# Kernel optimization log

Hardware: AMD Instinct MI355X
Metric: run time of the kernel (lower is better)

The kernel has to match this reference:

```python
import jax, jax.numpy as jnp
import numpy as np

B, P, ENC, DEC, ATT, EMB, V, CAPLEN = 128, 196, 2048, 512, 512, 300, 10000, 51


def setup_inputs() -> dict:
    key = jax.random.key(0)
    ks = jax.random.split(key, 20)
    s = 0.02
    lens = jax.random.randint(ks[2], (B, 1), 2, CAPLEN + 1)
    lens = lens.at[0, 0].set(CAPLEN)  # ensure max decode length == CAPLEN-1 (static T)
    return {
        'encoder_out': jax.random.normal(ks[0], (B, P, ENC), jnp.float32),
        'encoded_captions': jax.random.randint(ks[1], (B, CAPLEN), 0, V),
        'caption_lengths': lens,
        'W_enc_att': jax.random.normal(ks[3], (ATT, ENC)) * s,
        'b_enc_att': jnp.zeros((ATT,)),
        'W_dec_att': jax.random.normal(ks[4], (ATT, DEC)) * s,
        'b_dec_att': jnp.zeros((ATT,)),
        'w_full_att': jax.random.normal(ks[5], (ATT,)) * s,
        'b_full_att': jnp.zeros(()),
        'embedding': jax.random.uniform(ks[6], (V, EMB), minval=-0.1, maxval=0.1),
        'W_ih': jax.random.normal(ks[7], (4 * DEC, EMB + ENC)) * s,
        'b_ih': jnp.zeros((4 * DEC,)),
        'W_hh': jax.random.normal(ks[8], (4 * DEC, DEC)) * s,
        'b_hh': jnp.zeros((4 * DEC,)),
        'W_init_h': jax.random.normal(ks[9], (DEC, ENC)) * s,
        'b_init_h': jnp.zeros((DEC,)),
        'W_init_c': jax.random.normal(ks[10], (DEC, ENC)) * s,
        'b_init_c': jnp.zeros((DEC,)),
        'W_fbeta': jax.random.normal(ks[11], (ENC, DEC)) * s,
        'b_fbeta': jnp.zeros((ENC,)),
        'W_fc': jax.random.uniform(ks[12], (V, DEC), minval=-0.1, maxval=0.1),
        'b_fc': jnp.zeros((V,)),
    }


def reference(encoder_out, encoded_captions, caption_lengths,
              W_enc_att, b_enc_att, W_dec_att, b_dec_att, w_full_att, b_full_att,
              embedding, W_ih, b_ih, W_hh, b_hh,
              W_init_h, b_init_h, W_init_c, b_init_c,
              W_fbeta, b_fbeta, W_fc, b_fc):
    lens = caption_lengths[:, 0]
    sort_ind = jnp.argsort(-lens)                      # descending length sort
    lens_s = lens[sort_ind]
    enc = encoder_out[sort_ind]                        # [B,P,ENC]
    caps = encoded_captions[sort_ind]                  # [B,CAPLEN]
    emb = embedding[caps]                              # [B,CAPLEN,EMB]
    mean_enc = enc.mean(axis=1)
    h0 = mean_enc @ W_init_h.T + b_init_h
    c0 = mean_enc @ W_init_c.T + b_init_c
    att1 = enc @ W_enc_att.T + b_enc_att               # precomputed [B,P,ATT]
    decode_lengths = lens_s - 1
    T = caps.shape[1] - 1                              # static max decode length
    mask = jnp.arange(T)[:, None] < decode_lengths[None, :]   # [T,B]
    emb_t = jnp.transpose(emb[:, :T, :], (1, 0, 2))    # [T,B,EMB]

    def step(carry, xs):
        h, c = carry
        e_t, m_t = xs
        att2 = h @ W_dec_att.T + b_dec_att             # [B,ATT]
        score = jnp.einsum('bpa,a->bp', jax.nn.relu(att1 + att2[:, None, :]), w_full_att) + b_full_att
        alpha = jax.nn.softmax(score, axis=1)          # [B,P]
        awe = jnp.einsum('bp,bpe->be', alpha, enc)     # [B,ENC]
        gate = jax.nn.sigmoid(h @ W_fbeta.T + b_fbeta)
        awe = gate * awe
        x = jnp.concatenate([e_t, awe], axis=1)        # [B,EMB+ENC]
        gates = x @ W_ih.T + b_ih + h @ W_hh.T + b_hh
        i, f, g, o = jnp.split(gates, 4, axis=1)
        i, f, o = jax.nn.sigmoid(i), jax.nn.sigmoid(f), jax.nn.sigmoid(o)
        g = jnp.tanh(g)
        c_new = f * c + i * g
        h_new = o * jnp.tanh(c_new)
        m = m_t[:, None]
        # state only advances for still-active (length > t) rows
        h2 = jnp.where(m, h_new, h)
        c2 = jnp.where(m, c_new, c)
        preds = h_new @ W_fc.T + b_fc                  # dropout is identity in eval
        preds = jnp.where(m, preds, 0.0)
        alpha = jnp.where(m, alpha, 0.0)
        return (h2, c2), (preds, alpha)

    (_, _), (preds, alphas) = jax.lax.scan(step, (h0, c0), (emb_t, mask))
    predictions = jnp.transpose(preds, (1, 0, 2))      # [B,T,V]
    alphas = jnp.transpose(alphas, (1, 0, 2))          # [B,T,P]
    return predictions, caps, decode_lengths, alphas, sort_ind
```

## Files before the change

kernel.cpp:

```cpp
#include <hip/hip_runtime.h>
#include <math.h>

#define B 128
#define PP 196
#define ENC 2048
#define DEC 512
#define ATTD 512
#define EMB 300
#define VV 10000
#define CAPLEN 51
#define TT 50
#define KPAD 2880
#define NPPAD 10112

static const long long OFF_PRED = 0LL;
static const long long OFF_CAPS = 64000000LL;
static const long long OFF_DECL = 64006528LL;
static const long long OFF_ALPH = 64006656LL;
static const long long OFF_SORT = 65261056LL;

typedef unsigned short ushort_t;
typedef unsigned int uint_t;
typedef short bf8 __attribute__((ext_vector_type(8)));
typedef float f4 __attribute__((ext_vector_type(4)));

__device__ __forceinline__ float sigf(float x){ return 1.f/(1.f+expf(-x)); }
__device__ __forceinline__ float b2f(ushort_t u){
  union{uint_t i; float f;} v; v.i = ((uint_t)u)<<16; return v.f;
}
__device__ __forceinline__ ushort_t f2b(float f){
  union{float f; uint_t i;} v; v.f = f;
  uint_t r = v.i + 0x7fffu + ((v.i>>16)&1u);
  return (ushort_t)(r>>16);
}
__device__ __forceinline__ uint_t pack2(float lo, float hi){
  return (uint_t)f2b(lo) | ((uint_t)f2b(hi)<<16);
}
__device__ __forceinline__ float2 b2x2(uint_t u){
  union{uint_t i; float f;} a,b; a.i = u<<16; b.i = u & 0xffff0000u;
  return make_float2(a.f, b.f);
}

__device__ __forceinline__ void gemm128x64(
    const ushort_t* __restrict__ Ab, int lda, int m0,
    const ushort_t* __restrict__ Bb, int ldb, int n0,
    int Kbeg, int Kend, int mbound,
    ushort_t* As, ushort_t* Bs, int tid, f4 acc[4][2])
{
  const int r = tid>>2, cby = (tid&3)*8;
  const int w = tid>>6, l = tid&63;
  const int wm = w>>1, wn = w&1, lr = l&15, lk = (l>>4)*8;
  uint4 qa0 = *(const uint4*)(Ab + (size_t)(m0+r)*lda    + Kbeg + cby);
  uint4 qa1 = *(const uint4*)(Ab + (size_t)(m0+64+r)*lda + Kbeg + cby);
  uint4 qb  = *(const uint4*)(Bb + (size_t)(n0+r)*ldb    + Kbeg + cby);
  for (int k0=Kbeg; k0<Kend; k0+=32){
    __syncthreads();
    *(uint4*)(As + r*40      + cby) = qa0;
    *(uint4*)(As + (64+r)*40 + cby) = qa1;
    *(uint4*)(Bs + r*40      + cby) = qb;
    __syncthreads();
    if (k0+32 < Kend){
      qa0 = *(const uint4*)(Ab + (size_t)(m0+r)*lda    + k0+32 + cby);
      qa1 = *(const uint4*)(Ab + (size_t)(m0+64+r)*lda + k0+32 + cby);
      qb  = *(const uint4*)(Bb + (size_t)(n0+r)*ldb    + k0+32 + cby);
    }
    bf8 b0 = *(const bf8*)(Bs + (wn*32+lr)*40    + lk);
    bf8 b1 = *(const bf8*)(Bs + (wn*32+16+lr)*40 + lk);
    #pragma unroll
    for (int fm=0; fm<4; fm++){
      if (wm*64 + fm*16 < mbound){
        bf8 a = *(const bf8*)(As + (wm*64+fm*16+lr)*40 + lk);
        acc[fm][0] = __builtin_amdgcn_mfma_f32_16x16x32_bf16(a, b0, acc[fm][0], 0, 0, 0);
        acc[fm][1] = __builtin_amdgcn_mfma_f32_16x16x32_bf16(a, b1, acc[fm][1], 0, 0, 0);
      }
    }
  }
}

__global__ __launch_bounds__(128) void k_prep(const int* __restrict__ cap_len,
    const int* __restrict__ enc_caps, float* __restrict__ out,
    int* __restrict__ sort_i, int* __restrict__ decl_i, int* __restrict__ caps_i,
    int* __restrict__ nact_d){
  __shared__ int lens[B];
  __shared__ int sind[B];
  __shared__ int s_dl[B];
  int t = threadIdx.x;
  lens[t] = cap_len[t];
  __syncthreads();
  int my = lens[t];
  int rank = 0;
  for (int j=0;j<B;j++){
    int lj = lens[j];
    if (lj > my || (lj == my && j < t)) rank++;
  }
  sind[rank] = t;
  __syncthreads();
  int src = sind[t];
  sort_i[t] = src;
  int dl = lens[src]-1;
  decl_i[t] = dl;
  s_dl[t] = dl;
  out[OFF_DECL+t] = (float)dl;
  out[OFF_SORT+t] = (float)src;
  for (int j=0;j<CAPLEN;j++){
    int v = enc_caps[src*CAPLEN+j];
    caps_i[t*CAPLEN+j] = v;
    out[OFF_CAPS + t*CAPLEN + j] = (float)v;
  }
  __syncthreads();
  if (t < TT){
    int cnt = 0;
    for (int b2=0;b2<B;b2++) cnt += (s_dl[b2] > t) ? 1 : 0;
    nact_d[t] = cnt;
  }
}

__global__ __launch_bounds__(256) void k_mean(const float* __restrict__ enc,
    const int* __restrict__ sort_i, float* __restrict__ meanb){
  int b = blockIdx.x;
  int e = blockIdx.y*256 + threadIdx.x;
  int sb = sort_i[b];
  const float* p0 = enc + (size_t)sb*PP*ENC + e;
  float s = 0.f;
  for (int p=0;p<PP;p++) s += p0[(size_t)p*ENC];
  meanb[b*ENC+e] = s * (1.0f/PP);
}

__global__ __launch_bounds__(256) void k_init(const float* __restrict__ meanb,
    const float* __restrict__ Wh, const float* __restrict__ bh,
    const float* __restrict__ Wc, const float* __restrict__ bc,
    float* __restrict__ h, float* __restrict__ c, ushort_t* __restrict__ xb_s){
  __shared__ float aT[64*132];
  __shared__ float wT[64*36];
  int tid = threadIdx.x;
  int n0 = blockIdx.x*32;
  const float* Wm  = blockIdx.y ? Wc : Wh;
  const float* bia = blockIdx.y ? bc : bh;
  float* dst = blockIdx.y ? c : h;
  int bt = tid&15, nt = tid>>4;
  float acc[8][2] = {};
  for (int k0=0;k0<ENC;k0+=64){
    for (int idx=tid; idx<64*128; idx+=256){
      int k=idx&63, m=idx>>6;
      aT[k*132+m] = meanb[m*ENC + k0+k];
    }
    for (int idx=tid; idx<64*32; idx+=256){
      int k=idx&63, n=idx>>6;
      wT[k*36+n] = Wm[(size_t)(n0+n)*ENC + k0+k];
    }
    __syncthreads();
    #pragma unroll 4
    for (int k=0;k<64;k++){
      float a[8], wv[2];
      *(float4*)&a[0] = *(const float4*)&aT[k*132+bt*8];
      *(float4*)&a[4] = *(const float4*)&aT[k*132+bt*8+4];
      *(float2*)&wv[0] = *(const float2*)&wT[k*36+nt*2];
      #pragma unroll
      for (int i=0;i<8;i++){ acc[i][0]+=a[i]*wv[0]; acc[i][1]+=a[i]*wv[1]; }
    }
    __syncthreads();
  }
  #pragma unroll
  for (int i=0;i<8;i++){
    int m = bt*8+i;
    #pragma unroll
    for (int j=0;j<2;j++){
      int n = n0+nt*2+j;
      float v = acc[i][j] + bia[n];
      dst[m*DEC+n] = v;
      if (blockIdx.y == 0) xb_s[(size_t)m*KPAD + n] = f2b(v);
    }
  }
}

__global__ __launch_bounds__(256) void k_wkb(const float* __restrict__ Whh,
    const float* __restrict__ Wih, uint_t* __restrict__ wkb_u){
  int n = blockIdx.x;
  int j = n>>2, g = n&3;
  int rrow = g*512 + j;
  uint_t* dst = wkb_u + (size_t)n*(KPAD/2);
  for (int u=threadIdx.x; u<KPAD/2; u+=256){
    int k = 2*u; float a, bvl;
    if (k < 512){ float2 v = *(const float2*)(Whh + (size_t)rrow*512 + k); a=v.x; bvl=v.y; }
    else if (k < 2860){ float2 v = *(const float2*)(Wih + (size_t)rrow*2348 + (k-512)); a=v.x; bvl=v.y; }
    else { a=0.f; bvl=0.f; }
    dst[u] = pack2(a, bvl);
  }
}
__global__ __launch_bounds__(256) void k_wcatb(const float* __restrict__ Wda,
    const float* __restrict__ Wfb, uint_t* __restrict__ wcat_u){
  int n = blockIdx.x;
  const float* src = (n < 512) ? (Wda + (size_t)n*512) : (Wfb + (size_t)(n-512)*512);
  uint_t* dst = wcat_u + (size_t)n*256;
  int u = threadIdx.x;
  float2 v = *(const float2*)(src + 2*u);
  dst[u] = pack2(v.x, v.y);
}
__global__ __launch_bounds__(256) void k_wfcb(const float* __restrict__ Wfc,
    uint_t* __restrict__ wfc_u){
  int n = blockIdx.x;
  uint_t* dst = wfc_u + (size_t)n*256;
  int u = threadIdx.x;
  if (n < VV){
    float2 v = *(const float2*)(Wfc + (size_t)n*512 + 2*u);
    dst[u] = pack2(v.x, v.y);
  } else dst[u] = 0u;
}
__global__ __launch_bounds__(256) void k_weab(const float* __restrict__ Wea,
    uint_t* __restrict__ wea_u){
  int n = blockIdx.x;
  uint_t* dst = wea_u + (size_t)n*1024;
  for (int u=threadIdx.x; u<1024; u+=256){
    float2 v = *(const float2*)(Wea + (size_t)n*2048 + 2*u);
    dst[u] = pack2(v.x, v.y);
  }
}
__global__ __launch_bounds__(160) void k_embb(const float* __restrict__ embedding,
    const int* __restrict__ caps_i, uint_t* __restrict__ embb_u){
  int b = blockIdx.x, t = blockIdx.y, tid = threadIdx.x;
  if (tid >= 150) return;
  int tok = caps_i[b*CAPLEN+t];
  float2 v = *(const float2*)(embedding + (size_t)tok*EMB + 2*tid);
  embb_u[((size_t)b*TT+t)*150 + tid] = pack2(v.x, v.y);
}
__global__ __launch_bounds__(256) void k_xpad(uint_t* __restrict__ xb_u){
  for (int u=threadIdx.x; u<1280; u+=256){
    int r = u/10, cu = u - r*10;
    xb_u[(size_t)r*(KPAD/2) + 1430 + cu] = 0u;
  }
}
__global__ __launch_bounds__(256) void k_encb(const float* __restrict__ enc,
    const int* __restrict__ sort_i, ushort_t* __restrict__ encb){
  int row = blockIdx.x;
  int b = row/PP, p = row - b*PP;
  int sb = sort_i[b];
  const float4* s4 = (const float4*)(enc + ((size_t)sb*PP+p)*ENC);
  uint4* d4 = (uint4*)(encb + (size_t)row*ENC);
  int tid = threadIdx.x;
  float4 f0 = s4[tid*2], f1 = s4[tid*2+1];
  uint4 q;
  q.x = pack2(f0.x,f0.y); q.y = pack2(f0.z,f0.w);
  q.z = pack2(f1.x,f1.y); q.w = pack2(f1.z,f1.w);
  d4[tid] = q;
}

__global__ __launch_bounds__(256) void k_zero(const int* __restrict__ decl_i,
    float* __restrict__ out){
  int blk = blockIdx.x;
  int b = blk/TT, t = blk - b*TT;
  if (t < decl_i[b]) return;
  float4 z = {0.f,0.f,0.f,0.f};
  float4* p = (float4*)(out + OFF_PRED + ((size_t)b*TT+t)*VV);
  for (int i=threadIdx.x; i<VV/4; i+=256) p[i] = z;
  size_t ao = (size_t)OFF_ALPH + ((size_t)b*TT+t)*PP;
  if (threadIdx.x < PP) out[ao + threadIdx.x] = 0.f;
}

__global__ __launch_bounds__(256) void k_att1g(const ushort_t* __restrict__ encb,
    const ushort_t* __restrict__ weab, const float* __restrict__ bea,
    ushort_t* __restrict__ attb){
  __shared__ ushort_t As[128*40];
  __shared__ ushort_t Bs[64*40];
  int tid = threadIdx.x;
  int m0 = blockIdx.x*128, n0 = blockIdx.y*64;
  f4 acc[4][2] = {};
  gemm128x64(encb, 2048, m0, weab, 2048, n0, 0, 2048, 128, As, Bs, tid, acc);
  int w = tid>>6, l = tid&63, wm = w>>1, wn = w&1;
  #pragma unroll
  for (int fm=0; fm<4; fm++)
    #pragma unroll
    for (int fn=0; fn<2; fn++)
      #pragma unroll
      for (int rr=0; rr<4; rr++){
        int m = m0 + wm*64 + fm*16 + (l>>4)*4 + rr;
        int n = n0 + wn*32 + fn*16 + (l&15);
        attb[(size_t)m*ATTD + n] = f2b(acc[fm][fn][rr] + bea[n]);
      }
}

__global__ __launch_bounds__(256) void k_att1_f32(const float* __restrict__ enc,
    const float* __restrict__ Wea, const float* __restrict__ bea,
    const int* __restrict__ sort_i, ushort_t* __restrict__ attb){
  __shared__ float aT[64*132];
  __shared__ float wT[64*68];
  int tid = threadIdx.x;
  int m0 = blockIdx.x*128;
  int n0 = blockIdx.y*64;
  int bt = tid&15, nt = tid>>4;
  float acc[8][4] = {};
  for (int k0=0;k0<ENC;k0+=64){
    for (int idx=tid; idx<64*128; idx+=256){
      int k=idx&63, m=idx>>6;
      int mg = m0+m;
      int b = mg/PP; int p = mg - b*PP;
      int sb = sort_i[b];
      aT[k*132+m] = enc[((size_t)sb*PP + p)*ENC + k0+k];
    }
    for (int idx=tid; idx<64*64; idx+=256){
      int k=idx&63, n=idx>>6;
      wT[k*68+n] = Wea[(size_t)(n0+n)*ENC + k0+k];
    }
    __syncthreads();
    #pragma unroll 4
    for (int k=0;k<64;k++){
      float a[8], wv[4];
      *(float4*)&a[0] = *(const float4*)&aT[k*132+bt*8];
      *(float4*)&a[4] = *(const float4*)&aT[k*132+bt*8+4];
      *(float4*)&wv[0] = *(const float4*)&wT[k*68+nt*4];
      #pragma unroll
      for (int i=0;i<8;i++)
        #pragma unroll
        for (int j=0;j<4;j++) acc[i][j] += a[i]*wv[j];
    }
    __syncthreads();
  }
  #pragma unroll
  for (int i=0;i<8;i++){
    int mg = m0+bt*8+i;
    #pragma unroll
    for (int j=0;j<4;j++){
      int n = n0+nt*4+j;
      attb[(size_t)mg*ATTD + n] = f2b(acc[i][j] + bea[n]);
    }
  }
}

__global__ __launch_bounds__(256) void k_hmats(const ushort_t* __restrict__ xb,
    const ushort_t* __restrict__ wcatb, const float* __restrict__ bda,
    const float* __restrict__ bfb, const int* __restrict__ nact_d,
    float* __restrict__ att2s, float* __restrict__ gate, int t){
  __shared__ ushort_t As[128*40];
  __shared__ ushort_t Bs[64*40];
  int tid = threadIdx.x;
  int n0 = blockIdx.x*64;
  int mb = nact_d[t];
  f4 acc[4][2] = {};
  gemm128x64(xb, KPAD, 0, wcatb, 512, n0, 0, 512, mb, As, Bs, tid, acc);
  int w = tid>>6, l = tid&63, wm = w>>1, wn = w&1;
  #pragma unroll
  for (int fm=0; fm<4; fm++)
    #pragma unroll
    for (int fn=0; fn<2; fn++)
      #pragma unroll
      for (int rr=0; rr<4; rr++){
        int m = wm*64 + fm*16 + (l>>4)*4 + rr;
        int n = n0 + wn*32 + fn*16 + (l&15);
        float v = acc[fm][fn][rr];
        if (n < 512) att2s[m*512+n] = v + bda[n];
        else         gate[m*2048 + (n-512)] = sigf(v + bfb[n-512]);
      }
}

template<bool FULLT>
__global__ __launch_bounds__(512) void k_score_awe(const ushort_t* __restrict__ attb,
    const float* __restrict__ att2s, const float* __restrict__ wfa,
    const float* __restrict__ bfa, const int* __restrict__ decl_i,
    const float* __restrict__ gate, const ushort_t* __restrict__ encb,
    const float* __restrict__ enc, const int* __restrict__ sort_i,
    float* __restrict__ out, uint_t* __restrict__ xb_u,
    const uint_t* __restrict__ embb_u, const float* __restrict__ embedding,
    const int* __restrict__ caps_i, int t){
  int b = blockIdx.x, tid = threadIdx.x;
  if (t >= decl_i[b]) return;
  __shared__ float s_a2[512], s_w[512], s_sc[200], s_al[200], s_red[8], s_red2[8];
  if (FULLT){
    if (tid < 150) xb_u[b*(KPAD/2) + 256 + tid] = embb_u[((size_t)b*TT+t)*150 + tid];
  } else {
    if (tid < 150){
      int tok = caps_i[b*CAPLEN+t];
      float2 e = *(const float2*)(embedding + (size_t)tok*EMB + 2*tid);
      xb_u[b*(KPAD/2) + 256 + tid] = pack2(e.x, e.y);
    }
  }
  s_a2[tid] = att2s[b*512+tid];
  s_w[tid]  = wfa[tid];
  __syncthreads();
  int wid = tid>>6, lane = tid&63;
  float b0 = bfa[0];
  for (int p=wid; p<PP; p+=8){
    uint4 q = ((const uint4*)(attb + ((size_t)b*PP + p)*ATTD))[lane];
    int j = lane*8;
    float2 x0=b2x2(q.x), x1=b2x2(q.y), x2=b2x2(q.z), x3=b2x2(q.w);
    float s = fmaxf(x0.x+s_a2[j+0],0.f)*s_w[j+0] + fmaxf(x0.y+s_a2[j+1],0.f)*s_w[j+1]
            + fmaxf(x1.x+s_a2[j+2],0.f)*s_w[j+2] + fmaxf(x1.y+s_a2[j+3],0.f)*s_w[j+3]
            + fmaxf(x2.x+s_a2[j+4],0.f)*s_w[j+4] + fmaxf(x2.y+s_a2[j+5],0.f)*s_w[j+5]
            + fmaxf(x3.x+s_a2[j+6],0.f)*s_w[j+6] + fmaxf(x3.y+s_a2[j+7],0.f)*s_w[j+7];
    #pragma unroll
    for (int off=32;off;off>>=1) s += __shfl_down(s,off);
    if (lane==0) s_sc[p] = s + b0;
  }
  __syncthreads();
  float sc = (tid<PP) ? s_sc[tid] : -1e30f;
  float mx = sc;
  #pragma unroll
  for (int off=32;off;off>>=1) mx = fmaxf(mx, __shfl_down(mx,off));
  if (lane==0) s_red[wid] = mx;
  __syncthreads();
  mx = s_red[0];
  #pragma unroll
  for (int i=1;i<8;i++) mx = fmaxf(mx, s_red[i]);
  float e = (tid<PP) ? expf(sc-mx) : 0.f;
  float sm = e;
  #pragma unroll
  for (int off=32;off;off>>=1) sm += __shfl_down(sm,off);
  if (lane==0) s_red2[wid] = sm;
  __syncthreads();
  float tot = 0.f;
  #pragma unroll
  for (int i=0;i<8;i++) tot += s_red2[i];
  float inv = 1.f/tot;
  if (tid<PP){
    float al = e*inv;
    s_al[tid] = al;
    out[(size_t)OFF_ALPH + ((size_t)b*TT+t)*PP + tid] = al;
  }
  __syncthreads();
  float a0=0.f,a1=0.f,a2=0.f,a3=0.f;
  if (FULLT){
    const uint2* E = (const uint2*)(encb + (size_t)b*PP*ENC) + tid;
    #pragma unroll 4
    for (int p=0;p<PP;p++){
      float al = s_al[p];
      uint2 q = E[(size_t)p*(ENC/4)];
      float2 u = b2x2(q.x), v = b2x2(q.y);
      a0 += al*u.x; a1 += al*u.y; a2 += al*v.x; a3 += al*v.y;
    }
  } else {
    const float4* E = (const float4*)(enc + (size_t)sort_i[b]*PP*ENC) + tid;
    #pragma unroll 4
    for (int p=0;p<PP;p++){
      float al = s_al[p];
      float4 q = E[(size_t)p*(ENC/4)];
      a0 += al*q.x; a1 += al*q.y; a2 += al*q.z; a3 += al*q.w;
    }
  }
  float4 g = *(const float4*)(gate + b*2048 + tid*4);
  xb_u[b*(KPAD/2) + 406 + tid*2]     = pack2(a0*g.x, a1*g.y);
  xb_u[b*(KPAD/2) + 406 + tid*2 + 1] = pack2(a2*g.z, a3*g.w);
}

__global__ __launch_bounds__(256) void k_b1gf(const ushort_t* __restrict__ xb,
    const ushort_t* __restrict__ wkbi, const float* __restrict__ b_ih,
    const float* __restrict__ b_hh, const int* __restrict__ decl_i,
    const int* __restrict__ nact_d, float* __restrict__ c,
    ushort_t* __restrict__ hnball, ushort_t* __restrict__ xb_s, int t){
  __shared__ ushort_t As[128*40];
  __shared__ ushort_t Bs[64*40];
  __shared__ float sacc[128*68];
  __shared__ float sbias[64];
  __shared__ int s_dl[128];
  int tid = threadIdx.x;
  int n0 = blockIdx.x*64;
  int j0 = n0>>2;
  int mb = nact_d[t];
  if (tid < 64){
    int n = n0 + tid;
    int j = n>>2, g = n&3;
    sbias[tid] = b_ih[g*512+j] + b_hh[g*512+j];
  }
  if (tid < 128) s_dl[tid] = decl_i[tid];
  f4 acc[4][2] = {};
  gemm128x64(xb, KPAD, 0, wkbi, KPAD, n0, 0, KPAD, mb, As, Bs, tid, acc);
  int w = tid>>6, l = tid&63, wm = w>>1, wn = w&1;
  __syncthreads();
  #pragma unroll
  for (int fm=0; fm<4; fm++)
    #pragma unroll
    for (int fn=0; fn<2; fn++)
      #pragma unroll
      for (int rr=0; rr<4; rr++){
        int m = wm*64 + fm*16 + (l>>4)*4 + rr;
        int n = wn*32 + fn*16 + (l&15);
        sacc[m*68+n] = acc[fm][fn][rr];
      }
  __syncthreads();
  #pragma unroll
  for (int q=0; q<8; q++){
    int idx = q*256 + tid;
    int m = idx>>4, u = idx&15;
    int j = j0 + u;
    float gi = sacc[m*68 + u*4+0] + sbias[u*4+0];
    float gf = sacc[m*68 + u*4+1] + sbias[u*4+1];
    float gg = sacc[m*68 + u*4+2] + sbias[u*4+2];
    float go = sacc[m*68 + u*4+3] + sbias[u*4+3];
    float cn = sigf(gf)*c[m*512+j] + sigf(gi)*tanhf(gg);
    float hn = sigf(go)*tanhf(cn);
    hnball[((size_t)t*B + m)*512 + j] = f2b(hn);
    if (t < s_dl[m]){
      c[m*512+j] = cn;
      xb_s[(size_t)m*KPAD + j] = f2b(hn);
    }
  }
}

__global__ __launch_bounds__(256) void k_predall(const ushort_t* __restrict__ hnball,
    const ushort_t* __restrict__ wfcb, const float* __restrict__ b_fc,
    const int* __restrict__ nact_d, float* __restrict__ out){
  __shared__ ushort_t As[128*40];
  __shared__ ushort_t Bs[64*40];
  int tid = threadIdx.x;
  int t = blockIdx.y;
  int n0 = blockIdx.x*64;
  int mb = nact_d[t];
  f4 acc[4][2] = {};
  gemm128x64(hnball + (size_t)t*B*512, 512, 0, wfcb, 512, n0, 0, 512, mb, As, Bs, tid, acc);
  int w = tid>>6, l = tid&63, wm = w>>1, wn = w&1;
  #pragma unroll
  for (int fm=0; fm<4; fm++)
    #pragma unroll
    for (int fn=0; fn<2; fn++)
      #pragma unroll
      for (int rr=0; rr<4; rr++){
        int m = wm*64 + fm*16 + (l>>4)*4 + rr;
        int n = n0 + wn*32 + fn*16 + (l&15);
        if (m < mb && n < VV)
          out[OFF_PRED + ((size_t)m*TT + t)*VV + n] = acc[fm][fn][rr] + b_fc[n];
      }
}

extern "C" void kernel_launch(void* const* d_in, const int* in_sizes, int n_in,
                              void* d_out, int out_size, void* d_ws, size_t ws_size,
                              hipStream_t stream){
  const float* enc       = (const float*)d_in[0];
  const int*   caps_in   = (const int*)d_in[1];
  const int*   caplen    = (const int*)d_in[2];
  const float* W_enc_att = (const float*)d_in[3];
  const float* b_enc_att = (const float*)d_in[4];
  const float* W_dec_att = (const float*)d_in[5];
  const float* b_dec_att = (const float*)d_in[6];
  const float* w_full_att= (const float*)d_in[7];
  const float* b_full_att= (const float*)d_in[8];
  const float* embedding = (const float*)d_in[9];
  const float* W_ih      = (const float*)d_in[10];
  const float* b_ih      = (const float*)d_in[11];
  const float* W_hh      = (const float*)d_in[12];
  const float* b_hh      = (const float*)d_in[13];
  const float* W_init_h  = (const float*)d_in[14];
  const float* b_init_h  = (const float*)d_in[15];
  const float* W_init_c  = (const float*)d_in[16];
  const float* b_init_c  = (const float*)d_in[17];
  const float* W_fbeta   = (const float*)d_in[18];
  const float* b_fbeta   = (const float*)d_in[19];
  const float* W_fc      = (const float*)d_in[20];
  const float* b_fc      = (const float*)d_in[21];
  float* out = (float*)d_out;

  float* W = (float*)d_ws;
  size_t o = 0;
  auto A = [&](size_t n){ float* p = W + o; o += n; return p; };

  bool FULL = ws_size >= 172000000ull;

  float* h      = A(65536);
  float* c      = A(65536);
  float* att2s  = A(65536);
  float* gate   = A(262144);
  float* meanb  = A(262144);
  ushort_t* xb    = (ushort_t*)A(184320);
  ushort_t* wkb   = (ushort_t*)A(2949120);
  ushort_t* wcatb = (ushort_t*)A(655360);
  ushort_t* wfcb  = (ushort_t*)A(2588672);
  ushort_t* hnball= (ushort_t*)A(1638400);
  ushort_t* attb  = (ushort_t*)A(6422528);
  int* ip = (int*)A(6848);
  int* sort_i = ip;
  int* decl_i = ip + 128;
  int* nact_d = ip + 256;
  int* caps_i = ip + 320;
  ushort_t* weab = nullptr;
  uint_t*   embb_u = nullptr;
  ushort_t* encb = nullptr;
  if (FULL){
    weab   = (ushort_t*)A(524288);
    embb_u = (uint_t*)A(960000);
    encb   = (ushort_t*)A(25690112);
  }
  uint_t* xb_u = (uint_t*)xb;

  k_prep<<<1,128,0,stream>>>(caplen, caps_in, out, sort_i, decl_i, caps_i, nact_d);
  k_mean<<<dim3(128,8),256,0,stream>>>(enc, sort_i, meanb);
  k_init<<<dim3(16,2),256,0,stream>>>(meanb, W_init_h, b_init_h, W_init_c, b_init_c, h, c, xb);
  k_wkb<<<2048,256,0,stream>>>(W_hh, W_ih, (uint_t*)wkb);
  k_wcatb<<<2560,256,0,stream>>>(W_dec_att, W_fbeta, (uint_t*)wcatb);
  k_wfcb<<<NPPAD,256,0,stream>>>(W_fc, (uint_t*)wfcb);
  k_xpad<<<1,256,0,stream>>>(xb_u);
  k_zero<<<6400,256,0,stream>>>(decl_i, out);
  if (FULL){
    k_weab<<<512,256,0,stream>>>(W_enc_att, (uint_t*)weab);
    k_embb<<<dim3(128,50),160,0,stream>>>(embedding, caps_i, embb_u);
    k_encb<<<25088,256,0,stream>>>(enc, sort_i, encb);
    k_att1g<<<dim3(196,8),256,0,stream>>>(encb, weab, b_enc_att, attb);
  } else {
    k_att1_f32<<<dim3(196,8),256,0,stream>>>(enc, W_enc_att, b_enc_att, sort_i, attb);
  }

  for (int t=0;t<TT;t++){
    k_hmats<<<40,256,0,stream>>>(xb, wcatb, b_dec_att, b_fbeta, nact_d, att2s, gate, t);
    if (FULL)
      k_score_awe<true><<<128,512,0,stream>>>(attb, att2s, w_full_att, b_full_att, decl_i,
          gate, encb, enc, sort_i, out, xb_u, embb_u, embedding, caps_i, t);
    else
      k_score_awe<false><<<128,512,0,stream>>>(attb, att2s, w_full_att, b_full_att, decl_i,
          gate, encb, enc, sort_i, out, xb_u, embb_u, embedding, caps_i, t);
    k_b1gf<<<32,256,0,stream>>>(xb, wkb, b_ih, b_hh, decl_i, nact_d, c, hnball, xb, t);
  }
  k_predall<<<dim3(158,TT),256,0,stream>>>(hnball, wfcb, b_fc, nact_d, out);
}
```

Measured before the change: 5.269 ms.

## Fuse per-step decoder loop into persistent kernel with grid barriers

Replaces the 150 per-timestep kernel launches with a single persistent kernel of 128 blocks that separates the hmats, score/awe and LSTM gate phases with atomic grid barriers, and double-buffers the x state. It also turns the init projection into a bf16 MFMA GEMM, widens GEMM K tiles from 32 to 64, computes the mean from the bf16 encoder copy, and folds the weight/embedding conversions into the consuming kernels. The goal is to remove launch overhead and inter-kernel gaps on the sequential critical path. The cost is spin barriers with a timeout guard that depend on all 128 blocks being co-resident, plus bf16 rounding of the mean.

Result: slower. 13.26 ms (+151.6%).

```diff
diff --git a/kernel.cpp b/kernel.cpp
--- a/kernel.cpp
+++ b/kernel.cpp
@@ -10,8 +10,10 @@
 #define VV 10000
 #define CAPLEN 51
 #define TT 50
-#define KPAD 2880
+#define KP3 3072
+#define KUSE 2880
 #define NPPAD 10112
+#define NBLK 128
 
 static const long long OFF_PRED = 0LL;
 static const long long OFF_CAPS = 64000000LL;
@@ -41,37 +43,59 @@
   return make_float2(a.f, b.f);
 }
 
-__device__ __forceinline__ void gemm128x64(
+__device__ __forceinline__ void gbar(int* bar, int target){
+  __syncthreads();
+  if (threadIdx.x == 0){
+    __hip_atomic_fetch_add(bar, 1, __ATOMIC_ACQ_REL, __HIP_MEMORY_SCOPE_AGENT);
+    int guard = 0;
+    while (__hip_atomic_load(bar, __ATOMIC_ACQUIRE, __HIP_MEMORY_SCOPE_AGENT) < target){
+      __builtin_amdgcn_s_sleep(8);
+      if (++guard > (1<<17)) break;
+    }
+  }
+  __syncthreads();
+}
+
+__device__ __forceinline__ void gemmBK64(
     const ushort_t* __restrict__ Ab, int lda, int m0,
     const ushort_t* __restrict__ Bb, int ldb, int n0,
     int Kbeg, int Kend, int mbound,
     ushort_t* As, ushort_t* Bs, int tid, f4 acc[4][2])
 {
-  const int r = tid>>2, cby = (tid&3)*8;
+  const int r = tid>>3, c8 = (tid&7)*8;
   const int w = tid>>6, l = tid&63;
-  const int wm = w>>1, wn = w&1, lr = l&15, lk = (l>>4)*8;
-  uint4 qa0 = *(const uint4*)(Ab + (size_t)(m0+r)*lda    + Kbeg + cby);
-  uint4 qa1 = *(const uint4*)(Ab + (size_t)(m0+64+r)*lda + Kbeg + cby);
-  uint4 qb  = *(const uint4*)(Bb + (size_t)(n0+r)*ldb    + Kbeg + cby);
-  for (int k0=Kbeg; k0<Kend; k0+=32){
+  const int wm = w>>1, wn = w&1, lr = l&15, lkq = (l>>4)*8;
+  uint4 pa[4], pb[2];
+  #pragma unroll
+  for (int j=0;j<4;j++) pa[j] = *(const uint4*)(Ab + (size_t)(m0 + r + j*32)*lda + Kbeg + c8);
+  #pragma unroll
+  for (int j=0;j<2;j++) pb[j] = *(const uint4*)(Bb + (size_t)(n0 + r + j*32)*ldb + Kbeg + c8);
+  for (int k0=Kbeg; k0<Kend; k0+=64){
     __syncthreads();
-    *(uint4*)(As + r*40      + cby) = qa0;
-    *(uint4*)(As + (64+r)*40 + cby) = qa1;
-    *(uint4*)(Bs + r*40      + cby) = qb;
+    #pragma unroll
+    for (int j=0;j<4;j++) *(uint4*)(As + (r+j*32)*72 + c8) = pa[j];
+    #pragma unroll
+    for (int j=0;j<2;j++) *(uint4*)(Bs + (r+j*32)*72 + c8) = pb[j];
     __syncthreads();
-    if (k0+32 < Kend){
-      qa0 = *(const uint4*)(Ab + (size_t)(m0+r)*lda    + k0+32 + cby);
-      qa1 = *(const uint4*)(Ab + (size_t)(m0+64+r)*lda + k0+32 + cby);
-      qb  = *(const uint4*)(Bb + (size_t)(n0+r)*ldb    + k0+32 + cby);
-    }
-    bf8 b0 = *(const bf8*)(Bs + (wn*32+lr)*40    + lk);
-    bf8 b1 = *(const bf8*)(Bs + (wn*32+16+lr)*40 + lk);
+    if (k0+64 < Kend){
+      #pragma unroll
+      for (int j=0;j<4;j++) pa[j] = *(const uint4*)(Ab + (size_t)(m0 + r + j*32)*lda + k0+64 + c8);
+      #pragma unroll
+      for (int j=0;j<2;j++) pb[j] = *(const uint4*)(Bb + (size_t)(n0 + r + j*32)*ldb + k0+64 + c8);
+    }
+    bf8 b00 = *(const bf8*)(Bs + (wn*32+lr)*72 + lkq);
+    bf8 b01 = *(const bf8*)(Bs + (wn*32+lr)*72 + lkq + 32);
+    bf8 b10 = *(const bf8*)(Bs + (wn*32+16+lr)*72 + lkq);
+    bf8 b11 = *(const bf8*)(Bs + (wn*32+16+lr)*72 + lkq + 32);
     #pragma unroll
     for (int fm=0; fm<4; fm++){
       if (wm*64 + fm*16 < mbound){
-        bf8 a = *(const bf8*)(As + (wm*64+fm*16+lr)*40 + lk);
-        acc[fm][0] = __builtin_amdgcn_mfma_f32_16x16x32_bf16(a, b0, acc[fm][0], 0, 0, 0);
-        acc[fm][1] = __builtin_amdgcn_mfma_f32_16x16x32_bf16(a, b1, acc[fm][1], 0, 0, 0);
+        bf8 a0 = *(const bf8*)(As + (wm*64+fm*16+lr)*72 + lkq);
+        bf8 a1 = *(const bf8*)(As + (wm*64+fm*16+lr)*72 + lkq + 32);
+        acc[fm][0] = __builtin_amdgcn_mfma_f32_16x16x32_bf16(a0, b00, acc[fm][0], 0,0,0);
+        acc[fm][0] = __builtin_amdgcn_mfma_f32_16x16x32_bf16(a1, b01, acc[fm][0], 0,0,0);
+        acc[fm][1] = __builtin_amdgcn_mfma_f32_16x16x32_bf16(a0, b10, acc[fm][1], 0,0,0);
+        acc[fm][1] = __builtin_amdgcn_mfma_f32_16x16x32_bf16(a1, b11, acc[fm][1], 0,0,0);
       }
     }
   }
@@ -80,11 +104,12 @@
 __global__ __launch_bounds__(128) void k_prep(const int* __restrict__ cap_len,
     const int* __restrict__ enc_caps, float* __restrict__ out,
     int* __restrict__ sort_i, int* __restrict__ decl_i, int* __restrict__ caps_i,
-    int* __restrict__ nact_d){
+    int* __restrict__ nact_d, int* __restrict__ bar){
   __shared__ int lens[B];
   __shared__ int sind[B];
   __shared__ int s_dl[B];
   int t = threadIdx.x;
+  if (t == 0) *bar = 0;
   lens[t] = cap_len[t];
   __syncthreads();
   int my = lens[t];
@@ -115,120 +140,6 @@
   }
 }
 
-__global__ __launch_bounds__(256) void k_mean(const float* __restrict__ enc,
-    const int* __restrict__ sort_i, float* __restrict__ meanb){
-  int b = blockIdx.x;
-  int e = blockIdx.y*256 + threadIdx.x;
-  int sb = sort_i[b];
-  const float* p0 = enc + (size_t)sb*PP*ENC + e;
-  float s = 0.f;
-  for (int p=0;p<PP;p++) s += p0[(size_t)p*ENC];
-  meanb[b*ENC+e] = s * (1.0f/PP);
-}
-
-__global__ __launch_bounds__(256) void k_init(const float* __restrict__ meanb,
-    const float* __restrict__ Wh, const float* __restrict__ bh,
-    const float* __restrict__ Wc, const float* __restrict__ bc,
-    float* __restrict__ h, float* __restrict__ c, ushort_t* __restrict__ xb_s){
-  __shared__ float aT[64*132];
-  __shared__ float wT[64*36];
-  int tid = threadIdx.x;
-  int n0 = blockIdx.x*32;
-  const float* Wm  = blockIdx.y ? Wc : Wh;
-  const float* bia = blockIdx.y ? bc : bh;
-  float* dst = blockIdx.y ? c : h;
-  int bt = tid&15, nt = tid>>4;
-  float acc[8][2] = {};
-  for (int k0=0;k0<ENC;k0+=64){
-    for (int idx=tid; idx<64*128; idx+=256){
-      int k=idx&63, m=idx>>6;
-      aT[k*132+m] = meanb[m*ENC + k0+k];
-    }
-    for (int idx=tid; idx<64*32; idx+=256){
-      int k=idx&63, n=idx>>6;
-      wT[k*36+n] = Wm[(size_t)(n0+n)*ENC + k0+k];
-    }
-    __syncthreads();
-    #pragma unroll 4
-    for (int k=0;k<64;k++){
-      float a[8], wv[2];
-      *(float4*)&a[0] = *(const float4*)&aT[k*132+bt*8];
-      *(float4*)&a[4] = *(const float4*)&aT[k*132+bt*8+4];
-      *(float2*)&wv[0] = *(const float2*)&wT[k*36+nt*2];
-      #pragma unroll
-      for (int i=0;i<8;i++){ acc[i][0]+=a[i]*wv[0]; acc[i][1]+=a[i]*wv[1]; }
-    }
-    __syncthreads();
-  }
-  #pragma unroll
-  for (int i=0;i<8;i++){
-    int m = bt*8+i;
-    #pragma unroll
-    for (int j=0;j<2;j++){
-      int n = n0+nt*2+j;
-      float v = acc[i][j] + bia[n];
-      dst[m*DEC+n] = v;
-      if (blockIdx.y == 0) xb_s[(size_t)m*KPAD + n] = f2b(v);
-    }
-  }
-}
-
-__global__ __launch_bounds__(256) void k_wkb(const float* __restrict__ Whh,
-    const float* __restrict__ Wih, uint_t* __restrict__ wkb_u){
-  int n = blockIdx.x;
-  int j = n>>2, g = n&3;
-  int rrow = g*512 + j;
-  uint_t* dst = wkb_u + (size_t)n*(KPAD/2);
-  for (int u=threadIdx.x; u<KPAD/2; u+=256){
-    int k = 2*u; float a, bvl;
-    if (k < 512){ float2 v = *(const float2*)(Whh + (size_t)rrow*512 + k); a=v.x; bvl=v.y; }
-    else if (k < 2860){ float2 v = *(const float2*)(Wih + (size_t)rrow*2348 + (k-512)); a=v.x; bvl=v.y; }
-    else { a=0.f; bvl=0.f; }
-    dst[u] = pack2(a, bvl);
-  }
-}
-__global__ __launch_bounds__(256) void k_wcatb(const float* __restrict__ Wda,
-    const float* __restrict__ Wfb, uint_t* __restrict__ wcat_u){
-  int n = blockIdx.x;
-  const float* src = (n < 512) ? (Wda + (size_t)n*512) : (Wfb + (size_t)(n-512)*512);
-  uint_t* dst = wcat_u + (size_t)n*256;
-  int u = threadIdx.x;
-  float2 v = *(const float2*)(src + 2*u);
-  dst[u] = pack2(v.x, v.y);
-}
-__global__ __launch_bounds__(256) void k_wfcb(const float* __restrict__ Wfc,
-    uint_t* __restrict__ wfc_u){
-  int n = blockIdx.x;
-  uint_t* dst = wfc_u + (size_t)n*256;
-  int u = threadIdx.x;
-  if (n < VV){
-    float2 v = *(const float2*)(Wfc + (size_t)n*512 + 2*u);
-    dst[u] = pack2(v.x, v.y);
-  } else dst[u] = 0u;
-}
-__global__ __launch_bounds__(256) void k_weab(const float* __restrict__ Wea,
-    uint_t* __restrict__ wea_u){
-  int n = blockIdx.x;
-  uint_t* dst = wea_u + (size_t)n*1024;
-  for (int u=threadIdx.x; u<1024; u+=256){
-    float2 v = *(const float2*)(Wea + (size_t)n*2048 + 2*u);
-    dst[u] = pack2(v.x, v.y);
-  }
-}
-__global__ __launch_bounds__(160) void k_embb(const float* __restrict__ embedding,
-    const int* __restrict__ caps_i, uint_t* __restrict__ embb_u){
-  int b = blockIdx.x, t = blockIdx.y, tid = threadIdx.x;
-  if (tid >= 150) return;
-  int tok = caps_i[b*CAPLEN+t];
-  float2 v = *(const float2*)(embedding + (size_t)tok*EMB + 2*tid);
-  embb_u[((size_t)b*TT+t)*150 + tid] = pack2(v.x, v.y);
-}
-__global__ __launch_bounds__(256) void k_xpad(uint_t* __restrict__ xb_u){
-  for (int u=threadIdx.x; u<1280; u+=256){
-    int r = u/10, cu = u - r*10;
-    xb_u[(size_t)r*(KPAD/2) + 1430 + cu] = 0u;
-  }
-}
 __global__ __launch_bounds__(256) void k_encb(const float* __restrict__ enc,
     const int* __restrict__ sort_i, ushort_t* __restrict__ encb){
   int row = blockIdx.x;
@@ -244,6 +155,132 @@
   d4[tid] = q;
 }
 
+template<bool FULLT>
+__global__ __launch_bounds__(256) void k_mean(const ushort_t* __restrict__ encb,
+    const float* __restrict__ enc, const int* __restrict__ sort_i,
+    ushort_t* __restrict__ meanb){
+  int b = blockIdx.x, tid = threadIdx.x;
+  int ch = tid*8;
+  float a[8] = {};
+  if (FULLT){
+    const ushort_t* E = encb + (size_t)b*PP*ENC + ch;
+    for (int p=0;p<PP;p++){
+      uint4 q = *(const uint4*)(E + (size_t)p*ENC);
+      float2 u0=b2x2(q.x),u1=b2x2(q.y),u2=b2x2(q.z),u3=b2x2(q.w);
+      a[0]+=u0.x; a[1]+=u0.y; a[2]+=u1.x; a[3]+=u1.y;
+      a[4]+=u2.x; a[5]+=u2.y; a[6]+=u3.x; a[7]+=u3.y;
+    }
+  } else {
+    const float* E = enc + ((size_t)sort_i[b]*PP)*ENC + ch;
+    for (int p=0;p<PP;p++){
+      float4 f0 = *(const float4*)(E + (size_t)p*ENC);
+      float4 f1 = *(const float4*)(E + (size_t)p*ENC + 4);
+      a[0]+=f0.x; a[1]+=f0.y; a[2]+=f0.z; a[3]+=f0.w;
+      a[4]+=f1.x; a[5]+=f1.y; a[6]+=f1.z; a[7]+=f1.w;
+    }
+  }
+  const float inv = 1.0f/PP;
+  uint4 q;
+  q.x = pack2(a[0]*inv, a[1]*inv); q.y = pack2(a[2]*inv, a[3]*inv);
+  q.z = pack2(a[4]*inv, a[5]*inv); q.w = pack2(a[6]*inv, a[7]*inv);
+  *(uint4*)( (uint_t*)meanb + (size_t)b*(ENC/2) + tid*4 ) = q;
+}
+
+__global__ __launch_bounds__(256) void k_initg(const ushort_t* __restrict__ meanb,
+    const float* __restrict__ Wh, const float* __restrict__ bh,
+    const float* __restrict__ Wc, const float* __restrict__ bc,
+    float* __restrict__ c, ushort_t* __restrict__ xb0){
+  __shared__ __align__(16) ushort_t As[128*72];
+  __shared__ __align__(16) ushort_t Bs[64*72];
+  int tid = threadIdx.x;
+  int n0 = blockIdx.x*64;
+  const int r = tid>>3, c8 = (tid&7)*8;
+  const int w = tid>>6, l = tid&63, wm = w>>1, wn = w&1, lr = l&15, lkq = (l>>4)*8;
+  f4 acc[4][2] = {};
+  for (int k0=0; k0<ENC; k0+=64){
+    __syncthreads();
+    #pragma unroll
+    for (int j=0;j<4;j++){
+      int rr = r + j*32;
+      *(uint4*)(As + rr*72 + c8) = *(const uint4*)(meanb + (size_t)rr*ENC + k0 + c8);
+    }
+    #pragma unroll
+    for (int j=0;j<2;j++){
+      int rr = r + j*32;
+      int n = n0 + rr;
+      const float* src = (n < 512) ? (Wh + (size_t)n*ENC + k0 + c8)
+                                   : (Wc + (size_t)(n-512)*ENC + k0 + c8);
+      float4 f0 = *(const float4*)src, f1 = *(const float4*)(src+4);
+      uint4 q; q.x=pack2(f0.x,f0.y); q.y=pack2(f0.z,f0.w); q.z=pack2(f1.x,f1.y); q.w=pack2(f1.z,f1.w);
+      *(uint4*)(Bs + rr*72 + c8) = q;
+    }
+    __syncthreads();
+    bf8 b00 = *(const bf8*)(Bs + (wn*32+lr)*72 + lkq);
+    bf8 b01 = *(const bf8*)(Bs + (wn*32+lr)*72 + lkq + 32);
+    bf8 b10 = *(const bf8*)(Bs + (wn*32+16+lr)*72 + lkq);
+    bf8 b11 = *(const bf8*)(Bs + (wn*32+16+lr)*72 + lkq + 32);
+    #pragma unroll
+    for (int fm=0; fm<4; fm++){
+      bf8 a0 = *(const bf8*)(As + (wm*64+fm*16+lr)*72 + lkq);
+      bf8 a1 = *(const bf8*)(As + (wm*64+fm*16+lr)*72 + lkq + 32);
+      acc[fm][0] = __builtin_amdgcn_mfma_f32_16x16x32_bf16(a0, b00, acc[fm][0], 0,0,0);
+      acc[fm][0] = __builtin_amdgcn_mfma_f32_16x16x32_bf16(a1, b01, acc[fm][0], 0,0,0);
+      acc[fm][1] = __builtin_amdgcn_mfma_f32_16x16x32_bf16(a0, b10, acc[fm][1], 0,0,0);
+      acc[fm][1] = __builtin_amdgcn_mfma_f32_16x16x32_bf16(a1, b11, acc[fm][1], 0,0,0);
+    }
+  }
+  #pragma unroll
+  for (int fm=0; fm<4; fm++)
+    #pragma unroll
+    for (int fn=0; fn<2; fn++)
+      #pragma unroll
+      for (int rr=0; rr<4; rr++){
+        int m = wm*64 + fm*16 + (l>>4)*4 + rr;
+        int n = n0 + wn*32 + fn*16 + (l&15);
+        float v = acc[fm][fn][rr];
+        if (n < 512) xb0[(size_t)m*KP3 + n] = f2b(v + bh[n]);
+        else         c[m*DEC + (n-512)] = v + bc[n-512];
+      }
+}
+
+__global__ __launch_bounds__(256) void k_wkbi(const float* __restrict__ Whh,
+    const float* __restrict__ Wih, uint_t* __restrict__ wkb_u){
+  int n = blockIdx.x;
+  int j = n>>2, g = n&3;
+  int srow = g*512 + j;
+  uint_t* dst = wkb_u + (size_t)n*(KP3/2);
+  for (int u=threadIdx.x; u<KP3/2; u+=256){
+    int k = 2*u; float a, bv;
+    if (k < 512){ float2 v = *(const float2*)(Whh + (size_t)srow*512 + k); a=v.x; bv=v.y; }
+    else if (k < 2860){ float2 v = *(const float2*)(Wih + (size_t)srow*2348 + (k-512)); a=v.x; bv=v.y; }
+    else { a=0.f; bv=0.f; }
+    dst[u] = pack2(a, bv);
+  }
+}
+__global__ __launch_bounds__(256) void k_wcatb(const float* __restrict__ Wda,
+    const float* __restrict__ Wfb, uint_t* __restrict__ wcat_u){
+  int n = blockIdx.x;
+  const float* src = (n < 512) ? (Wda + (size_t)n*512) : (Wfb + (size_t)(n-512)*512);
+  float2 v = *(const float2*)(src + 2*threadIdx.x);
+  wcat_u[(size_t)n*256 + threadIdx.x] = pack2(v.x, v.y);
+}
+__global__ __launch_bounds__(256) void k_wfcb(const float* __restrict__ Wfc,
+    uint_t* __restrict__ wfc_u){
+  int n = blockIdx.x;
+  if (n < VV){
+    float2 v = *(const float2*)(Wfc + (size_t)n*512 + 2*threadIdx.x);
+    wfc_u[(size_t)n*256 + threadIdx.x] = pack2(v.x, v.y);
+  } else wfc_u[(size_t)n*256 + threadIdx.x] = 0u;
+}
+__global__ __launch_bounds__(256) void k_xpad(uint_t* __restrict__ xb0_u,
+    uint_t* __restrict__ xb1_u){
+  uint_t* x = blockIdx.x ? xb1_u : xb0_u;
+  for (int idx=threadIdx.x; idx<128*106; idx+=256){
+    int rr = idx/106, cc = idx - rr*106;
+    x[(size_t)rr*(KP3/2) + 1430 + cc] = 0u;
+  }
+}
+
 __global__ __launch_bounds__(256) void k_zero(const int* __restrict__ decl_i,
     float* __restrict__ out){
   int blk = blockIdx.x;
@@ -256,16 +293,57 @@
   if (threadIdx.x < PP) out[ao + threadIdx.x] = 0.f;
 }
 
+template<bool FULLT>
 __global__ __launch_bounds__(256) void k_att1g(const ushort_t* __restrict__ encb,
-    const ushort_t* __restrict__ weab, const float* __restrict__ bea,
+    const float* __restrict__ enc, const int* __restrict__ sort_i,
+    const float* __restrict__ Wea, const float* __restrict__ bea,
     ushort_t* __restrict__ attb){
-  __shared__ ushort_t As[128*40];
-  __shared__ ushort_t Bs[64*40];
+  __shared__ __align__(16) ushort_t As[128*72];
+  __shared__ __align__(16) ushort_t Bs[64*72];
   int tid = threadIdx.x;
   int m0 = blockIdx.x*128, n0 = blockIdx.y*64;
+  const int r = tid>>3, c8 = (tid&7)*8;
+  const int w = tid>>6, l = tid&63, wm = w>>1, wn = w&1, lr = l&15, lkq = (l>>4)*8;
   f4 acc[4][2] = {};
-  gemm128x64(encb, 2048, m0, weab, 2048, n0, 0, 2048, 128, As, Bs, tid, acc);
-  int w = tid>>6, l = tid&63, wm = w>>1, wn = w&1;
+  for (int k0=0; k0<ENC; k0+=64){
+    __syncthreads();
+    #pragma unroll
+    for (int j=0;j<4;j++){
+      int rr = r + j*32, mg = m0 + rr;
+      uint4 q;
+      if (FULLT){
+        q = *(const uint4*)(encb + (size_t)mg*ENC + k0 + c8);
+      } else {
+        int bq = mg/PP, p = mg - bq*PP;
+        const float* src = enc + ((size_t)sort_i[bq]*PP + p)*ENC + k0 + c8;
+        float4 f0 = *(const float4*)src, f1 = *(const float4*)(src+4);
+        q.x=pack2(f0.x,f0.y); q.y=pack2(f0.z,f0.w); q.z=pack2(f1.x,f1.y); q.w=pack2(f1.z,f1.w);
+      }
+      *(uint4*)(As + rr*72 + c8) = q;
+    }
+    #pragma unroll
+    for (int j=0;j<2;j++){
+      int rr = r + j*32;
+      const float* src = Wea + (size_t)(n0+rr)*ENC + k0 + c8;
+      float4 f0 = *(const float4*)src, f1 = *(const float4*)(src+4);
+      uint4 q; q.x=pack2(f0.x,f0.y); q.y=pack2(f0.z,f0.w); q.z=pack2(f1.x,f1.y); q.w=pack2(f1.z,f1.w);
+      *(uint4*)(Bs + rr*72 + c8) = q;
+    }
+    __syncthreads();
+    bf8 b00 = *(const bf8*)(Bs + (wn*32+lr)*72 + lkq);
+    bf8 b01 = *(const bf8*)(Bs + (wn*32+lr)*72 + lkq + 32);
+    bf8 b10 = *(const bf8*)(Bs + (wn*32+16+lr)*72 + lkq);
+    bf8 b11 = *(const bf8*)(Bs + (wn*32+16+lr)*72 + lkq + 32);
+    #pragma unroll
+    for (int fm=0; fm<4; fm++){
+      bf8 a0 = *(const bf8*)(As + (wm*64+fm*16+lr)*72 + lkq);
+      bf8 a1 = *(const bf8*)(As + (wm*64+fm*16+lr)*72 + lkq + 32);
+      acc[fm][0] = __builtin_amdgcn_mfma_f32_16x16x32_bf16(a0, b00, acc[fm][0], 0,0,0);
+      acc[fm][0] = __builtin_amdgcn_mfma_f32_16x16x32_bf16(a1, b01, acc[fm][0], 0,0,0);
+      acc[fm][1] = __builtin_amdgcn_mfma_f32_16x16x32_bf16(a0, b10, acc[fm][1], 0,0,0);
+      acc[fm][1] = __builtin_amdgcn_mfma_f32_16x16x32_bf16(a1, b11, acc[fm][1], 0,0,0);
+    }
+  }
   #pragma unroll
   for (int fm=0; fm<4; fm++)
     #pragma unroll
@@ -278,232 +356,220 @@
       }
 }
 
-__global__ __launch_bounds__(256) void k_att1_f32(const float* __restrict__ enc,
-    const float* __restrict__ Wea, const float* __restrict__ bea,
-    const int* __restrict__ sort_i, ushort_t* __restrict__ attb){
-  __shared__ float aT[64*132];
-  __shared__ float wT[64*68];
-  int tid = threadIdx.x;
-  int m0 = blockIdx.x*128;
-  int n0 = blockIdx.y*64;
-  int bt = tid&15, nt = tid>>4;
-  float acc[8][4] = {};
-  for (int k0=0;k0<ENC;k0+=64){
-    for (int idx=tid; idx<64*128; idx+=256){
-      int k=idx&63, m=idx>>6;
-      int mg = m0+m;
-      int b = mg/PP; int p = mg - b*PP;
-      int sb = sort_i[b];
-      aT[k*132+m] = enc[((size_t)sb*PP + p)*ENC + k0+k];
-    }
-    for (int idx=tid; idx<64*64; idx+=256){
-      int k=idx&63, n=idx>>6;
-      wT[k*68+n] = Wea[(size_t)(n0+n)*ENC + k0+k];
-    }
-    __syncthreads();
-    #pragma unroll 4
-    for (int k=0;k<64;k++){
-      float a[8], wv[4];
-      *(float4*)&a[0] = *(const float4*)&aT[k*132+bt*8];
-      *(float4*)&a[4] = *(const float4*)&aT[k*132+bt*8+4];
-      *(float4*)&wv[0] = *(const float4*)&wT[k*68+nt*4];
-      #pragma unroll
-      for (int i=0;i<8;i++)
+template<bool FULLT>
+__global__ __launch_bounds__(256) void k_persist(
+    ushort_t* __restrict__ xb0, ushort_t* __restrict__ xb1,
+    const ushort_t* __restrict__ wkbi, const ushort_t* __restrict__ wcatb,
+    const ushort_t* __restrict__ attb, const ushort_t* __restrict__ encb,
+    const float* __restrict__ enc, const float* __restrict__ embedding,
+    const float* __restrict__ bda, const float* __restrict__ bfb,
+    const float* __restrict__ wfa, const float* __restrict__ bfa,
+    const float* __restrict__ b_ih, const float* __restrict__ b_hh,
+    const int* __restrict__ sort_i, const int* __restrict__ decl_i,
+    const int* __restrict__ caps_i, const int* __restrict__ nact_d,
+    float* __restrict__ att2s, float* __restrict__ gate,
+    float* __restrict__ c, ushort_t* __restrict__ hnball,
+    float* __restrict__ out, int* bar)
+{
+  __shared__ __align__(16) ushort_t As[128*72];
+  __shared__ __align__(16) ushort_t Bs[64*72];
+  __shared__ float s_bias[32];
+  int blk = blockIdx.x, tid = threadIdx.x;
+  int bno = 0;
+  const int w = tid>>6, l = tid&63, wm = w>>1, wn = w&1;
+
+  for (int t=0; t<TT; ++t){
+    int mb = nact_d[t];
+    ushort_t* xbc = (t&1) ? xb1 : xb0;
+    ushort_t* xbn = (t&1) ? xb0 : xb1;
+    uint_t* xbc_u = (uint_t*)xbc;
+    if (blk < 40){
+      f4 acc[4][2] = {};
+      gemmBK64(xbc, KP3, 0, wcatb, 512, blk*64, 0, 512, mb, As, Bs, tid, acc);
+      #pragma unroll
+      for (int fm=0; fm<4; fm++)
         #pragma unroll
-        for (int j=0;j<4;j++) acc[i][j] += a[i]*wv[j];
-    }
-    __syncthreads();
-  }
-  #pragma unroll
-  for (int i=0;i<8;i++){
-    int mg = m0+bt*8+i;
-    #pragma unroll
-    for (int j=0;j<4;j++){
-      int n = n0+nt*4+j;
-      attb[(size_t)mg*ATTD + n] = f2b(acc[i][j] + bea[n]);
-    }
-  }
-}
-
-__global__ __launch_bounds__(256) void k_hmats(const ushort_t* __restrict__ xb,
-    const ushort_t* __restrict__ wcatb, const float* __restrict__ bda,
-    const float* __restrict__ bfb, const int* __restrict__ nact_d,
-    float* __restrict__ att2s, float* __restrict__ gate, int t){
-  __shared__ ushort_t As[128*40];
-  __shared__ ushort_t Bs[64*40];
-  int tid = threadIdx.x;
-  int n0 = blockIdx.x*64;
-  int mb = nact_d[t];
-  f4 acc[4][2] = {};
-  gemm128x64(xb, KPAD, 0, wcatb, 512, n0, 0, 512, mb, As, Bs, tid, acc);
-  int w = tid>>6, l = tid&63, wm = w>>1, wn = w&1;
-  #pragma unroll
-  for (int fm=0; fm<4; fm++)
-    #pragma unroll
-    for (int fn=0; fn<2; fn++)
-      #pragma unroll
-      for (int rr=0; rr<4; rr++){
-        int m = wm*64 + fm*16 + (l>>4)*4 + rr;
-        int n = n0 + wn*32 + fn*16 + (l&15);
-        float v = acc[fm][fn][rr];
-        if (n < 512) att2s[m*512+n] = v + bda[n];
-        else         gate[m*2048 + (n-512)] = sigf(v + bfb[n-512]);
-      }
-}
-
-template<bool FULLT>
-__global__ __launch_bounds__(512) void k_score_awe(const ushort_t* __restrict__ attb,
-    const float* __restrict__ att2s, const float* __restrict__ wfa,
-    const float* __restrict__ bfa, const int* __restrict__ decl_i,
-    const float* __restrict__ gate, const ushort_t* __restrict__ encb,
-    const float* __restrict__ enc, const int* __restrict__ sort_i,
-    float* __restrict__ out, uint_t* __restrict__ xb_u,
-    const uint_t* __restrict__ embb_u, const float* __restrict__ embedding,
-    const int* __restrict__ caps_i, int t){
-  int b = blockIdx.x, tid = threadIdx.x;
-  if (t >= decl_i[b]) return;
-  __shared__ float s_a2[512], s_w[512], s_sc[200], s_al[200], s_red[8], s_red2[8];
-  if (FULLT){
-    if (tid < 150) xb_u[b*(KPAD/2) + 256 + tid] = embb_u[((size_t)b*TT+t)*150 + tid];
-  } else {
-    if (tid < 150){
+        for (int fn=0; fn<2; fn++)
+          #pragma unroll
+          for (int rr=0; rr<4; rr++){
+            int m = wm*64 + fm*16 + (l>>4)*4 + rr;
+            int n = blk*64 + wn*32 + fn*16 + (l&15);
+            float v = acc[fm][fn][rr];
+            if (n < 512) att2s[m*512+n] = v + bda[n];
+            else         gate[m*2048 + (n-512)] = sigf(v + bfb[n-512]);
+          }
+    } else if (blk < 104){
+      int b = (blk-40)*2 + (tid>>7);
       int tok = caps_i[b*CAPLEN+t];
-      float2 e = *(const float2*)(embedding + (size_t)tok*EMB + 2*tid);
-      xb_u[b*(KPAD/2) + 256 + tid] = pack2(e.x, e.y);
-    }
-  }
-  s_a2[tid] = att2s[b*512+tid];
-  s_w[tid]  = wfa[tid];
-  __syncthreads();
-  int wid = tid>>6, lane = tid&63;
-  float b0 = bfa[0];
-  for (int p=wid; p<PP; p+=8){
-    uint4 q = ((const uint4*)(attb + ((size_t)b*PP + p)*ATTD))[lane];
-    int j = lane*8;
-    float2 x0=b2x2(q.x), x1=b2x2(q.y), x2=b2x2(q.z), x3=b2x2(q.w);
-    float s = fmaxf(x0.x+s_a2[j+0],0.f)*s_w[j+0] + fmaxf(x0.y+s_a2[j+1],0.f)*s_w[j+1]
-            + fmaxf(x1.x+s_a2[j+2],0.f)*s_w[j+2] + fmaxf(x1.y+s_a2[j+3],0.f)*s_w[j+3]
-            + fmaxf(x2.x+s_a2[j+4],0.f)*s_w[j+4] + fmaxf(x2.y+s_a2[j+5],0.f)*s_w[j+5]
-            + fmaxf(x3.x+s_a2[j+6],0.f)*s_w[j+6] + fmaxf(x3.y+s_a2[j+7],0.f)*s_w[j+7];
-    #pragma unroll
-    for (int off=32;off;off>>=1) s += __shfl_down(s,off);
-    if (lane==0) s_sc[p] = s + b0;
-  }
-  __syncthreads();
-  float sc = (tid<PP) ? s_sc[tid] : -1e30f;
-  float mx = sc;
-  #pragma unroll
-  for (int off=32;off;off>>=1) mx = fmaxf(mx, __shfl_down(mx,off));
-  if (lane==0) s_red[wid] = mx;
-  __syncthreads();
-  mx = s_red[0];
-  #pragma unroll
-  for (int i=1;i<8;i++) mx = fmaxf(mx, s_red[i]);
-  float e = (tid<PP) ? expf(sc-mx) : 0.f;
-  float sm = e;
-  #pragma unroll
-  for (int off=32;off;off>>=1) sm += __shfl_down(sm,off);
-  if (lane==0) s_red2[wid] = sm;
-  __syncthreads();
-  float tot = 0.f;
-  #pragma unroll
-  for (int i=0;i<8;i++) tot += s_red2[i];
-  float inv = 1.f/tot;
-  if (tid<PP){
-    float al = e*inv;
-    s_al[tid] = al;
-    out[(size_t)OFF_ALPH + ((size_t)b*TT+t)*PP + tid] = al;
-  }
-  __syncthreads();
-  float a0=0.f,a1=0.f,a2=0.f,a3=0.f;
-  if (FULLT){
-    const uint2* E = (const uint2*)(encb + (size_t)b*PP*ENC) + tid;
-    #pragma unroll 4
-    for (int p=0;p<PP;p++){
-      float al = s_al[p];
-      uint2 q = E[(size_t)p*(ENC/4)];
-      float2 u = b2x2(q.x), v = b2x2(q.y);
-      a0 += al*u.x; a1 += al*u.y; a2 += al*v.x; a3 += al*v.y;
-    }
-  } else {
-    const float4* E = (const float4*)(enc + (size_t)sort_i[b]*PP*ENC) + tid;
-    #pragma unroll 4
-    for (int p=0;p<PP;p++){
-      float al = s_al[p];
-      float4 q = E[(size_t)p*(ENC/4)];
-      a0 += al*q.x; a1 += al*q.y; a2 += al*q.z; a3 += al*q.w;
-    }
-  }
-  float4 g = *(const float4*)(gate + b*2048 + tid*4);
-  xb_u[b*(KPAD/2) + 406 + tid*2]     = pack2(a0*g.x, a1*g.y);
-  xb_u[b*(KPAD/2) + 406 + tid*2 + 1] = pack2(a2*g.z, a3*g.w);
-}
-
-__global__ __launch_bounds__(256) void k_b1gf(const ushort_t* __restrict__ xb,
-    const ushort_t* __restrict__ wkbi, const float* __restrict__ b_ih,
-    const float* __restrict__ b_hh, const int* __restrict__ decl_i,
-    const int* __restrict__ nact_d, float* __restrict__ c,
-    ushort_t* __restrict__ hnball, ushort_t* __restrict__ xb_s, int t){
-  __shared__ ushort_t As[128*40];
-  __shared__ ushort_t Bs[64*40];
-  __shared__ float sacc[128*68];
-  __shared__ float sbias[64];
-  __shared__ int s_dl[128];
-  int tid = threadIdx.x;
-  int n0 = blockIdx.x*64;
-  int j0 = n0>>2;
-  int mb = nact_d[t];
-  if (tid < 64){
-    int n = n0 + tid;
-    int j = n>>2, g = n&3;
-    sbias[tid] = b_ih[g*512+j] + b_hh[g*512+j];
-  }
-  if (tid < 128) s_dl[tid] = decl_i[tid];
-  f4 acc[4][2] = {};
-  gemm128x64(xb, KPAD, 0, wkbi, KPAD, n0, 0, KPAD, mb, As, Bs, tid, acc);
-  int w = tid>>6, l = tid&63, wm = w>>1, wn = w&1;
-  __syncthreads();
-  #pragma unroll
-  for (int fm=0; fm<4; fm++)
-    #pragma unroll
-    for (int fn=0; fn<2; fn++)
-      #pragma unroll
-      for (int rr=0; rr<4; rr++){
-        int m = wm*64 + fm*16 + (l>>4)*4 + rr;
-        int n = wn*32 + fn*16 + (l&15);
-        sacc[m*68+n] = acc[fm][fn][rr];
-      }
-  __syncthreads();
-  #pragma unroll
-  for (int q=0; q<8; q++){
-    int idx = q*256 + tid;
-    int m = idx>>4, u = idx&15;
-    int j = j0 + u;
-    float gi = sacc[m*68 + u*4+0] + sbias[u*4+0];
-    float gf = sacc[m*68 + u*4+1] + sbias[u*4+1];
-    float gg = sacc[m*68 + u*4+2] + sbias[u*4+2];
-    float go = sacc[m*68 + u*4+3] + sbias[u*4+3];
-    float cn = sigf(gf)*c[m*512+j] + sigf(gi)*tanhf(gg);
-    float hn = sigf(go)*tanhf(cn);
-    hnball[((size_t)t*B + m)*512 + j] = f2b(hn);
-    if (t < s_dl[m]){
-      c[m*512+j] = cn;
-      xb_s[(size_t)m*KPAD + j] = f2b(hn);
-    }
+      for (int u=(tid&127); u<150; u+=128){
+        float2 e = *(const float2*)(embedding + (size_t)tok*EMB + 2*u);
+        xbc_u[b*(KP3/2) + 256 + u] = pack2(e.x, e.y);
+      }
+    }
+    gbar(bar, (++bno)*NBLK);
+    {
+      int b = blk;
+      if (t < decl_i[b]){
+        float* sf   = (float*)As;
+        float* s_a2 = sf;          float* s_w  = sf+512;
+        float* s_sc = sf+1024;     float* s_al = sf+1232;
+        float* s_r1 = sf+1440;     float* s_r2 = sf+1448;
+        s_a2[tid] = att2s[b*512+tid]; s_a2[256+tid] = att2s[b*512+256+tid];
+        s_w[tid]  = wfa[tid];         s_w[256+tid]  = wfa[256+tid];
+        __syncthreads();
+        int wid = tid>>6, lane = tid&63;
+        float b0 = bfa[0];
+        for (int p=wid; p<PP; p+=4){
+          uint4 q = ((const uint4*)(attb + ((size_t)b*PP + p)*ATTD))[lane];
+          int j = lane*8;
+          float2 x0=b2x2(q.x), x1=b2x2(q.y), x2=b2x2(q.z), x3=b2x2(q.w);
+          float s = fmaxf(x0.x+s_a2[j+0],0.f)*s_w[j+0] + fmaxf(x0.y+s_a2[j+1],0.f)*s_w[j+1]
+                  + fmaxf(x1.x+s_a2[j+2],0.f)*s_w[j+2] + fmaxf(x1.y+s_a2[j+3],0.f)*s_w[j+3]
+                  + fmaxf(x2.x+s_a2[j+4],0.f)*s_w[j+4] + fmaxf(x2.y+s_a2[j+5],0.f)*s_w[j+5]
+                  + fmaxf(x3.x+s_a2[j+6],0.f)*s_w[j+6] + fmaxf(x3.y+s_a2[j+7],0.f)*s_w[j+7];
+          #pragma unroll
+          for (int off=32;off;off>>=1) s += __shfl_down(s,off);
+          if (lane==0) s_sc[p] = s + b0;
+        }
+        __syncthreads();
+        float sc = (tid<PP) ? s_sc[tid] : -1e30f;
+        float mx = sc;
+        #pragma unroll
+        for (int off=32;off;off>>=1) mx = fmaxf(mx, __shfl_down(mx,off));
+        if (lane==0) s_r1[wid] = mx;
+        __syncthreads();
+        mx = fmaxf(fmaxf(s_r1[0],s_r1[1]), fmaxf(s_r1[2],s_r1[3]));
+        float e = (tid<PP) ? expf(sc-mx) : 0.f;
+        float sm = e;
+        #pragma unroll
+        for (int off=32;off;off>>=1) sm += __shfl_down(sm,off);
+        if (lane==0) s_r2[wid] = sm;
+        __syncthreads();
+        float inv = 1.f/(s_r2[0]+s_r2[1]+s_r2[2]+s_r2[3]);
+        if (tid<PP){
+          float al = e*inv;
+          s_al[tid] = al;
+          out[(size_t)OFF_ALPH + ((size_t)b*TT+t)*PP + tid] = al;
+        }
+        __syncthreads();
+        int ch = tid*8;
+        float a0=0.f,a1=0.f,a2=0.f,a3=0.f,a4=0.f,a5=0.f,a6=0.f,a7=0.f;
+        if (FULLT){
+          const ushort_t* E = encb + (size_t)b*PP*ENC + ch;
+          #pragma unroll 2
+          for (int p=0;p<PP;p++){
+            uint4 q = *(const uint4*)(E + (size_t)p*ENC);
+            float al = s_al[p];
+            float2 u0=b2x2(q.x),u1=b2x2(q.y),u2=b2x2(q.z),u3=b2x2(q.w);
+            a0+=al*u0.x; a1+=al*u0.y; a2+=al*u1.x; a3+=al*u1.y;
+            a4+=al*u2.x; a5+=al*u2.y; a6+=al*u3.x; a7+=al*u3.y;
+          }
+        } else {
+          const float* E = enc + ((size_t)sort_i[b]*PP)*ENC + ch;
+          #pragma unroll 2
+          for (int p=0;p<PP;p++){
+            float4 f0 = *(const float4*)(E + (size_t)p*ENC);
+            float4 f1 = *(const float4*)(E + (size_t)p*ENC + 4);
+            float al = s_al[p];
+            a0+=al*f0.x; a1+=al*f0.y; a2+=al*f0.z; a3+=al*f0.w;
+            a4+=al*f1.x; a5+=al*f1.y; a6+=al*f1.z; a7+=al*f1.w;
+          }
+        }
+        float4 g0 = *(const float4*)(gate + b*2048 + ch);
+        float4 g1 = *(const float4*)(gate + b*2048 + ch + 4);
+        uint2 w0, w1;
+        w0.x = pack2(a0*g0.x, a1*g0.y); w0.y = pack2(a2*g0.z, a3*g0.w);
+        w1.x = pack2(a4*g1.x, a5*g1.y); w1.y = pack2(a6*g1.z, a7*g1.w);
+        *(uint2*)(xbc_u + b*(KP3/2) + 406 + tid*4)     = w0;
+        *(uint2*)(xbc_u + b*(KP3/2) + 406 + tid*4 + 2) = w1;
+      }
+    }
+    gbar(bar, (++bno)*NBLK);
+    if (blk < 64){
+      int n0q = blk*32;
+      if (tid < 32){
+        int g = tid&3, j = blk*8 + (tid>>2);
+        s_bias[tid] = b_ih[g*512+j] + b_hh[g*512+j];
+      }
+      const int r = tid>>3, c8 = (tid&7)*8;
+      const int lr = l&15, lkq = (l>>4)*8;
+      f4 acc[2][2] = {};
+      uint4 pa[4], pb1;
+      #pragma unroll
+      for (int j=0;j<4;j++) pa[j] = *(const uint4*)(xbc + (size_t)(r + j*32)*KP3 + c8);
+      pb1 = *(const uint4*)(wkbi + (size_t)(n0q + r)*KP3 + c8);
+      for (int k0=0; k0<KUSE; k0+=64){
+        __syncthreads();
+        #pragma unroll
+        for (int j=0;j<4;j++) *(uint4*)(As + (r+j*32)*72 + c8) = pa[j];
+        *(uint4*)(Bs + r*72 + c8) = pb1;
+        __syncthreads();
+        if (k0+64 < KUSE){
+          #pragma unroll
+          for (int j=0;j<4;j++) pa[j] = *(const uint4*)(xbc + (size_t)(r + j*32)*KP3 + k0+64 + c8);
+          pb1 = *(const uint4*)(wkbi + (size_t)(n0q + r)*KP3 + k0+64 + c8);
+        }
+        bf8 b00 = *(const bf8*)(Bs + lr*72 + lkq);
+        bf8 b01 = *(const bf8*)(Bs + lr*72 + lkq + 32);
+        bf8 b10 = *(const bf8*)(Bs + (16+lr)*72 + lkq);
+        bf8 b11 = *(const bf8*)(Bs + (16+lr)*72 + lkq + 32);
+        #pragma unroll
+        for (int fm=0; fm<2; fm++){
+          if (w*32 + fm*16 < mb){
+            bf8 a0 = *(const bf8*)(As + (w*32+fm*16+lr)*72 + lkq);
+            bf8 a1 = *(const bf8*)(As + (w*32+fm*16+lr)*72 + lkq + 32);
+            acc[fm][0] = __builtin_amdgcn_mfma_f32_16x16x32_bf16(a0, b00, acc[fm][0], 0,0,0);
+            acc[fm][0] = __builtin_amdgcn_mfma_f32_16x16x32_bf16(a1, b01, acc[fm][0], 0,0,0);
+            acc[fm][1] = __builtin_amdgcn_mfma_f32_16x16x32_bf16(a0, b10, acc[fm][1], 0,0,0);
+            acc[fm][1] = __builtin_amdgcn_mfma_f32_16x16x32_bf16(a1, b11, acc[fm][1], 0,0,0);
+          }
+        }
+      }
+      __syncthreads();
+      float* sacc = (float*)As;
+      #pragma unroll
+      for (int fm=0; fm<2; fm++)
+        #pragma unroll
+        for (int fn=0; fn<2; fn++)
+          #pragma unroll
+          for (int rr=0; rr<4; rr++){
+            int m = w*32 + fm*16 + (l>>4)*4 + rr;
+            int nn = fn*16 + (l&15);
+            sacc[m*33+nn] = acc[fm][fn][rr];
+          }
+      __syncthreads();
+      #pragma unroll
+      for (int q=0;q<4;q++){
+        int idx = q*256 + tid;
+        int m = idx>>3, u = idx&7;
+        int j = blk*8 + u;
+        float gi = sacc[m*33 + u*4+0] + s_bias[u*4+0];
+        float gf = sacc[m*33 + u*4+1] + s_bias[u*4+1];
+        float gg = sacc[m*33 + u*4+2] + s_bias[u*4+2];
+        float go = sacc[m*33 + u*4+3] + s_bias[u*4+3];
+        float cn = sigf(gf)*c[m*DEC+j] + sigf(gi)*tanhf(gg);
+        float hn = sigf(go)*tanhf(cn);
+        hnball[((size_t)t*B + m)*DEC + j] = f2b(hn);
+        bool act = t < decl_i[m];
+        if (act) c[m*DEC+j] = cn;
+        xbn[(size_t)m*KP3 + j] = act ? f2b(hn) : xbc[(size_t)m*KP3 + j];
+      }
+    }
+    gbar(bar, (++bno)*NBLK);
   }
 }
 
 __global__ __launch_bounds__(256) void k_predall(const ushort_t* __restrict__ hnball,
     const ushort_t* __restrict__ wfcb, const float* __restrict__ b_fc,
     const int* __restrict__ nact_d, float* __restrict__ out){
-  __shared__ ushort_t As[128*40];
-  __shared__ ushort_t Bs[64*40];
+  __shared__ __align__(16) ushort_t As[128*72];
+  __shared__ __align__(16) ushort_t Bs[64*72];
   int tid = threadIdx.x;
   int t = blockIdx.y;
   int n0 = blockIdx.x*64;
   int mb = nact_d[t];
   f4 acc[4][2] = {};
-  gemm128x64(hnball + (size_t)t*B*512, 512, 0, wfcb, 512, n0, 0, 512, mb, As, Bs, tid, acc);
+  gemmBK64(hnball + (size_t)t*B*DEC, DEC, 0, wfcb, DEC, n0, 0, DEC, mb, As, Bs, tid, acc);
   int w = tid>>6, l = tid&63, wm = w>>1, wn = w&1;
   #pragma unroll
   for (int fm=0; fm<4; fm++)
@@ -545,64 +611,51 @@
   const float* b_fc      = (const float*)d_in[21];
   float* out = (float*)d_out;
 
-  float* W = (float*)d_ws;
-  size_t o = 0;
-  auto A = [&](size_t n){ float* p = W + o; o += n; return p; };
-
-  bool FULL = ws_size >= 172000000ull;
-
-  float* h      = A(65536);
-  float* c      = A(65536);
-  float* att2s  = A(65536);
-  float* gate   = A(262144);
-  float* meanb  = A(262144);
-  ushort_t* xb    = (ushort_t*)A(184320);
-  ushort_t* wkb   = (ushort_t*)A(2949120);
-  ushort_t* wcatb = (ushort_t*)A(655360);
-  ushort_t* wfcb  = (ushort_t*)A(2588672);
-  ushort_t* hnball= (ushort_t*)A(1638400);
-  ushort_t* attb  = (ushort_t*)A(6422528);
-  int* ip = (int*)A(6848);
-  int* sort_i = ip;
-  int* decl_i = ip + 128;
-  int* nact_d = ip + 256;
-  int* caps_i = ip + 320;
-  ushort_t* weab = nullptr;
-  uint_t*   embb_u = nullptr;
-  ushort_t* encb = nullptr;
-  if (FULL){
-    weab   = (ushort_t*)A(524288);
-    embb_u = (uint_t*)A(960000);
-    encb   = (ushort_t*)A(25690112);
-  }
-  uint_t* xb_u = (uint_t*)xb;
-
-  k_prep<<<1,128,0,stream>>>(caplen, caps_in, out, sort_i, decl_i, caps_i, nact_d);
-  k_mean<<<dim3(128,8),256,0,stream>>>(enc, sort_i, meanb);
-  k_init<<<dim3(16,2),256,0,stream>>>(meanb, W_init_h, b_init_h, W_init_c, b_init_c, h, c, xb);
-  k_wkb<<<2048,256,0,stream>>>(W_hh, W_ih, (uint_t*)wkb);
+  char* base = (char*)d_ws;
+  size_t off = 0;
+  auto AL = [&](size_t bytes)->void*{ void* p = base + off; off = (off + bytes + 15) & ~15ull; return p; };
+
+  bool FULL = ws_size >= 168000000ull;
+
+  float* c      = (float*)AL(65536*4);
+  float* att2s  = (float*)AL(65536*4);
+  float* gate   = (float*)AL(262144*4);
+  ushort_t* meanb  = (ushort_t*)AL(262144*2);
+  ushort_t* xb0    = (ushort_t*)AL(393216*2);
+  ushort_t* xb1    = (ushort_t*)AL(393216*2);
+  ushort_t* wkbi   = (ushort_t*)AL((size_t)6291456*2);
+  ushort_t* wcatb  = (ushort_t*)AL(1310720*2);
+  ushort_t* wfcb   = (ushort_t*)AL(5177344*2);
+  ushort_t* hnball = (ushort_t*)AL(3276800*2);
+  ushort_t* attb   = (ushort_t*)AL((size_t)12845056*2);
+  int* sort_i = (int*)AL(128*4);
+  int* decl_i = (int*)AL(128*4);
+  int* nact_d = (int*)AL(64*4);
+  int* caps_i = (int*)AL(6528*4);
+  int* bar    = (int*)AL(64*4);
+  ushort_t* encb = FULL ? (ushort_t*)AL((size_t)51380224*2) : nullptr;
+
+  k_prep<<<1,128,0,stream>>>(caplen, caps_in, out, sort_i, decl_i, caps_i, nact_d, bar);
+  if (FULL) k_encb<<<25088,256,0,stream>>>(enc, sort_i, encb);
+  if (FULL) k_mean<true><<<128,256,0,stream>>>(encb, enc, sort_i, meanb);
+  else      k_mean<false><<<128,256,0,stream>>>(encb, enc, sort_i, meanb);
+  k_initg<<<16,256,0,stream>>>(meanb, W_init_h, b_init_h, W_init_c, b_init_c, c, xb0);
+  k_wkbi<<<2048,256,0,stream>>>(W_hh, W_ih, (uint_t*)wkbi);
   k_wcatb<<<2560,256,0,stream>>>(W_dec_att, W_fbeta, (uint_t*)wcatb);
   k_wfcb<<<NPPAD,256,0,stream>>>(W_fc, (uint_t*)wfcb);
-  k_xpad<<<1,256,0,stream>>>(xb_u);
+  k_xpad<<<2,256,0,stream>>>((uint_t*)xb0, (uint_t*)xb1);
   k_zero<<<6400,256,0,stream>>>(decl_i, out);
-  if (FULL){
-    k_weab<<<512,256,0,stream>>>(W_enc_att, (uint_t*)weab);
-    k_embb<<<dim3(128,50),160,0,stream>>>(embedding, caps_i, embb_u);
-    k_encb<<<25088,256,0,stream>>>(enc, sort_i, encb);
-    k_att1g<<<dim3(196,8),256,0,stream>>>(encb, weab, b_enc_att, attb);
-  } else {
-    k_att1_f32<<<dim3(196,8),256,0,stream>>>(enc, W_enc_att, b_enc_att, sort_i, attb);
-  }
-
-  for (int t=0;t<TT;t++){
-    k_hmats<<<40,256,0,stream>>>(xb, wcatb, b_dec_att, b_fbeta, nact_d, att2s, gate, t);
-    if (FULL)
-      k_score_awe<true><<<128,512,0,stream>>>(attb, att2s, w_full_att, b_full_att, decl_i,
-          gate, encb, enc, sort_i, out, xb_u, embb_u, embedding, caps_i, t);
-    else
-      k_score_awe<false><<<128,512,0,stream>>>(attb, att2s, w_full_att, b_full_att, decl_i,
-          gate, encb, enc, sort_i, out, xb_u, embb_u, embedding, caps_i, t);
-    k_b1gf<<<32,256,0,stream>>>(xb, wkb, b_ih, b_hh, decl_i, nact_d, c, hnball, xb, t);
-  }
+  if (FULL) k_att1g<true><<<dim3(196,8),256,0,stream>>>(encb, enc, sort_i, W_enc_att, b_enc_att, attb);
+  else      k_att1g<false><<<dim3(196,8),256,0,stream>>>(encb, enc, sort_i, W_enc_att, b_enc_att, attb);
+
+  if (FULL)
+    k_persist<true><<<NBLK,256,0,stream>>>(xb0, xb1, wkbi, wcatb, attb, encb, enc, embedding,
+        b_dec_att, b_fbeta, w_full_att, b_full_att, b_ih, b_hh,
+        sort_i, decl_i, caps_i, nact_d, att2s, gate, c, hnball, out, bar);
+  else
+    k_persist<false><<<NBLK,256,0,stream>>>(xb0, xb1, wkbi, wcatb, attb, encb, enc, embedding,
+        b_dec_att, b_fbeta, w_full_att, b_full_att, b_ih, b_hh,
+        sort_i, decl_i, caps_i, nact_d, att2s, gate, c, hnball, out, bar);
+
   k_predall<<<dim3(158,TT),256,0,stream>>>(hnball, wfcb, b_fc, nact_d, out);
 }
```
